# Kernel optimization log

Hardware: AMD Instinct MI355X
Metric: run time of the kernel (lower is better)

## Reference

```python
import jax, jax.numpy as jnp
import numpy as np

B, C, N, H = 16, 512, 4096, 512  # batch, visual_channels, visual_flat, hidden_size


def setup_inputs() -> dict:
    key = jax.random.key(0)
    kx, k1, k2, k3, k4 = jax.random.split(key, 5)
    stdv = 1.0 / np.sqrt(H)  # reset_parameters: uniform(-1/sqrt(size(0)), ...), size(0)=H for all weights
    u = lambda k, shape: jax.random.uniform(k, shape, jnp.float32, -stdv, stdv)
    return {
        "visual_inputs": jax.random.normal(kx, (B, C, N), jnp.float32),
        "w_cf": u(k1, (H, N)),  # channel_f: Linear(visual_flat -> hidden)
        "w_cg": u(k2, (H, N)),  # channel_g
        "w_sf": u(k3, (H, C)),  # spatial_f: Conv1d(C -> H, k=1), squeezed
        "w_sg": u(k4, (H, C)),  # spatial_g
    }


def reference(visual_inputs, w_cf, w_cg, w_sf, w_sg):
    x = visual_inputs  # [B, C, N]
    # ---- channel branch: sim[b,c,c'] = <cf[b,c,:], cg[b,c',:]>; summed over dim c then softmax over c'
    cf = jnp.einsum('bcn,hn->bch', x, w_cf)          # [B, C, H]
    cg = jnp.einsum('bcn,hn->bch', x, w_cg)          # [B, C, H]
    # sum_c sim[b,c,c'] = (sum_c cf[b,c,:]) . cg[b,c',:]  -- avoids [B,C,C]
    ch_comp = jnp.einsum('bh,bch->bc', cf.sum(axis=1), cg)        # [B, C]
    channel_mask = jax.nn.softmax(ch_comp, axis=1)[:, :, None]     # [B, C, 1]
    # ---- spatial branch: sim[b,i,j] = <sf[b,:,i], sg[b,:,j]>; summed over dim i then softmax over j
    sf = jnp.einsum('bcn,hc->bhn', x, w_sf)          # [B, H, N]
    sg = jnp.einsum('bcn,hc->bhn', x, w_sg)          # [B, H, N]
    sp_comp = jnp.einsum('bh,bhn->bn', sf.sum(axis=2), sg)         # [B, N]
    spatial_mask = jax.nn.softmax(sp_comp, axis=1)[:, None, :]     # [B, 1, N]
    outputs = x * channel_mask * spatial_mask        # [B, C, N]
    return outputs, channel_mask, spatial_mask
```

## Files before the change

### kernel.cpp

```cpp
#include <hip/hip_runtime.h>

#define Bq 16
#define Cq 512
#define Nq 4096
#define Hq 512

__global__ __launch_bounds__(256) void k1_xs(const float* __restrict__ x,
                                             float* __restrict__ xs_n,
                                             float* __restrict__ xs_c){
  __shared__ float lds[4];
  int blk = blockIdx.x;
  if (blk < Bq*4*4) {
    int b  = blk >> 4;
    int r  = blk & 15;
    int nc = r >> 2;
    int cc = r & 3;
    int n0 = nc*1024 + (int)threadIdx.x*4;
    const float4* px = (const float4*)(x + ((size_t)b*Cq + (size_t)cc*128)*Nq + n0);
    float4 acc = {0.f,0.f,0.f,0.f};
    #pragma unroll 4
    for (int c = 0; c < 128; ++c){
      float4 v = *px; px += Nq/4;
      acc.x += v.x; acc.y += v.y; acc.z += v.z; acc.w += v.w;
    }
    float* dst = xs_n + (size_t)b*Nq + n0;
    atomicAdd(dst+0, acc.x); atomicAdd(dst+1, acc.y);
    atomicAdd(dst+2, acc.z); atomicAdd(dst+3, acc.w);
  } else {
    int blk2 = blk - Bq*4*4;
    int b = blk2 >> 9;
    int c = blk2 & 511;
    const float4* row = (const float4*)(x + ((size_t)b*Cq + c)*Nq);
    float acc = 0.f;
    #pragma unroll
    for (int s = 0; s < 4; ++s){
      float4 v = row[s*256 + threadIdx.x];
      acc += (v.x + v.y) + (v.z + v.w);
    }
    #pragma unroll
    for (int off=32; off; off>>=1) acc += __shfl_down(acc, off, 64);
    if ((threadIdx.x & 63) == 0) lds[threadIdx.x >> 6] = acc;
    __syncthreads();
    if (threadIdx.x == 0) xs_c[b*Cq + c] = (lds[0]+lds[1])+(lds[2]+lds[3]);
  }
}

__global__ __launch_bounds__(256) void k2_s(const float* __restrict__ w_cf,
                                            const float* __restrict__ w_sf,
                                            const float* __restrict__ xs_n,
                                            const float* __restrict__ xs_c,
                                            float* __restrict__ s_cf,
                                            float* __restrict__ s_sf){
  __shared__ float lds[4];
  int blk = blockIdx.x;
  const float* w; const float* src; float* dst; int L;
  if (blk < Hq) { w = w_cf + (size_t)blk*Nq; src = xs_n; dst = s_cf; L = Nq; }
  else          { w = w_sf + (size_t)(blk-Hq)*Cq; src = xs_c; dst = s_sf; L = Cq; }
  int h = blk & (Hq-1);
  float acc[Bq];
  #pragma unroll
  for (int b=0;b<Bq;b++) acc[b]=0.f;
  for (int i = threadIdx.x; i < L; i += 256){
    float wv = w[i];
    #pragma unroll
    for (int b=0;b<Bq;b++) acc[b] += wv * src[b*L + i];
  }
  #pragma unroll
  for (int b=0;b<Bq;b++){
    float v = acc[b];
    #pragma unroll
    for (int off=32; off; off>>=1) v += __shfl_down(v, off, 64);
    if ((threadIdx.x & 63)==0) lds[threadIdx.x>>6] = v;
    __syncthreads();
    if (threadIdx.x==0) dst[b*Hq + h] = (lds[0]+lds[1])+(lds[2]+lds[3]);
    __syncthreads();
  }
}

__global__ __launch_bounds__(256) void k3_v(const float* __restrict__ w_cg,
                                            const float* __restrict__ w_sg,
                                            const float* __restrict__ s_cf,
                                            const float* __restrict__ s_sf,
                                            float* __restrict__ v_cg,
                                            float* __restrict__ v_sg){
  __shared__ float sl[Bq*64];
  int blk = blockIdx.x;
  const float* w; const float* s; float* dst; int L, jc, hc;
  if (blk < 128){ w=w_cg; s=s_cf; dst=v_cg; L=Nq; jc=blk>>3; hc=blk&7; }
  else { int k=blk-128; w=w_sg; s=s_sf; dst=v_sg; L=Cq; jc=k>>3; hc=k&7; }
  int h0 = hc*64;
  for (int i = threadIdx.x; i < Bq*64; i += 256){
    int b = i >> 6, hh = i & 63;
    sl[i] = s[b*Hq + h0 + hh];
  }
  __syncthreads();
  int j = (jc<<8) + (int)threadIdx.x;
  float acc[Bq];
  #pragma unroll
  for (int b=0;b<Bq;b++) acc[b]=0.f;
  for (int hh=0; hh<64; ++hh){
    float wv = w[(size_t)(h0+hh)*L + j];
    #pragma unroll
    for (int b=0;b<Bq;b++) acc[b] += sl[b*64+hh]*wv;
  }
  #pragma unroll
  for (int b=0;b<Bq;b++) atomicAdd(&dst[b*L + j], acc[b]);
}

__global__ __launch_bounds__(256) void k4_comp(const float* __restrict__ x,
                                               const float* __restrict__ v_cg,
                                               const float* __restrict__ v_sg,
                                               float* __restrict__ sp,
                                               float* __restrict__ ch){
  __shared__ float lds[4];
  int blk = blockIdx.x;
  if (blk < Bq*4*4){
    int b = blk >> 4; int r = blk & 15; int nc = r>>2; int cc = r&3;
    int n0 = nc*1024 + (int)threadIdx.x*4;
    const float4* px = (const float4*)(x + ((size_t)b*Cq + (size_t)cc*128)*Nq + n0);
    const float* vs = v_sg + b*Cq + cc*128;
    float4 acc = {0.f,0.f,0.f,0.f};
    #pragma unroll 4
    for (int c=0;c<128;++c){
      float4 v = *px; px += Nq/4;
      float s = vs[c];
      acc.x += v.x*s; acc.y += v.y*s; acc.z += v.z*s; acc.w += v.w*s;
    }
    float* dst = sp + (size_t)b*Nq + n0;
    atomicAdd(dst+0, acc.x); atomicAdd(dst+1, acc.y);
    atomicAdd(dst+2, acc.z); atomicAdd(dst+3, acc.w);
  } else {
    int blk2 = blk - Bq*4*4;
    int b = blk2 >> 9; int c = blk2 & 511;
    const float4* row = (const float4*)(x + ((size_t)b*Cq + c)*Nq);
    const float4* vg = (const float4*)(v_cg + (size_t)b*Nq);
    float acc=0.f;
    #pragma unroll
    for (int s=0;s<4;++s){
      float4 xv = row[s*256 + threadIdx.x];
      float4 vv = vg [s*256 + threadIdx.x];
      acc += xv.x*vv.x + xv.y*vv.y + xv.z*vv.z + xv.w*vv.w;
    }
    #pragma unroll
    for (int off=32; off; off>>=1) acc += __shfl_down(acc, off, 64);
    if ((threadIdx.x&63)==0) lds[threadIdx.x>>6]=acc;
    __syncthreads();
    if (threadIdx.x==0) ch[b*Cq+c] = (lds[0]+lds[1])+(lds[2]+lds[3]);
  }
}

__global__ __launch_bounds__(256) void k5_softmax(const float* __restrict__ ch,
                                                  const float* __restrict__ sp,
                                                  float* __restrict__ out){
  __shared__ float lds[4];
  __shared__ float bcast;
  int blk = blockIdx.x;
  const float* src; float* dst; int L;
  const size_t OUT0 = (size_t)Bq*Cq*Nq;
  if (blk < Bq){ int b=blk;    src=ch+(size_t)b*Cq; dst=out+OUT0+(size_t)b*Cq; L=Cq; }
  else         { int b=blk-Bq; src=sp+(size_t)b*Nq; dst=out+OUT0+(size_t)Bq*Cq+(size_t)b*Nq; L=Nq; }
  float m = -3.4e38f;
  for (int i=threadIdx.x;i<L;i+=256) m = fmaxf(m, src[i]);
  #pragma unroll
  for (int off=32; off; off>>=1) m = fmaxf(m, __shfl_down(m, off, 64));
  if ((threadIdx.x&63)==0) lds[threadIdx.x>>6]=m;
  __syncthreads();
  if (threadIdx.x==0) bcast = fmaxf(fmaxf(lds[0],lds[1]),fmaxf(lds[2],lds[3]));
  __syncthreads();
  m = bcast;
  float ssum=0.f;
  for (int i=threadIdx.x;i<L;i+=256) ssum += __expf(src[i]-m);
  #pragma unroll
  for (int off=32; off; off>>=1) ssum += __shfl_down(ssum, off, 64);
  __syncthreads();
  if ((threadIdx.x&63)==0) lds[threadIdx.x>>6]=ssum;
  __syncthreads();
  if (threadIdx.x==0) bcast = 1.f/((lds[0]+lds[1])+(lds[2]+lds[3]));
  __syncthreads();
  float inv = bcast;
  for (int i=threadIdx.x;i<L;i+=256) dst[i] = __expf(src[i]-m)*inv;
}

__global__ __launch_bounds__(256) void k6_out(const float* __restrict__ x,
                                              float* __restrict__ out){
  const size_t OUT0 = (size_t)Bq*Cq*Nq;
  const float* cm = out + OUT0;
  const float* sm = out + OUT0 + (size_t)Bq*Cq;
  int blk = blockIdx.x;
  int b = blk >> 11;
  int r = blk & 2047;
  int c = r >> 2;
  int q = r & 3;
  size_t rowoff = ((size_t)b*Cq + c)*Nq;
  int n0 = q*1024 + (int)threadIdx.x*4;
  float4 xv = *(const float4*)(x + rowoff + n0);
  float4 sv = *(const float4*)(sm + (size_t)b*Nq + n0);
  float cmv = cm[b*Cq + c];
  float4 o;
  o.x = xv.x*cmv*sv.x; o.y = xv.y*cmv*sv.y;
  o.z = xv.z*cmv*sv.z; o.w = xv.w*cmv*sv.w;
  *(float4*)(out + rowoff + n0) = o;
}

extern "C" void kernel_launch(void* const* d_in, const int* in_sizes, int n_in,
                              void* d_out, int out_size, void* d_ws, size_t ws_size,
                              hipStream_t stream){
  const float* x    = (const float*)d_in[0];
  const float* w_cf = (const float*)d_in[1];
  const float* w_cg = (const float*)d_in[2];
  const float* w_sf = (const float*)d_in[3];
  const float* w_sg = (const float*)d_in[4];
  float* out = (float*)d_out;

  float* ws   = (float*)d_ws;
  float* xs_n = ws;
  float* xs_c = xs_n + Bq*Nq;
  float* s_cf = xs_c + Bq*Cq;
  float* s_sf = s_cf + Bq*Hq;
  float* v_cg = s_sf + Bq*Hq;
  float* v_sg = v_cg + Bq*Nq;
  float* chc  = v_sg + Bq*Cq;
  float* spc  = chc  + Bq*Cq;

  size_t zbytes = (size_t)((spc + Bq*Nq) - ws) * sizeof(float);
  if (zbytes > ws_size) zbytes = ws_size;
  hipMemsetAsync(d_ws, 0, zbytes, stream);

  k1_xs     <<<Bq*4*4 + Bq*Cq, 256, 0, stream>>>(x, xs_n, xs_c);
  k2_s      <<<2*Hq,           256, 0, stream>>>(w_cf, w_sf, xs_n, xs_c, s_cf, s_sf);
  k3_v      <<<144,            256, 0, stream>>>(w_cg, w_sg, s_cf, s_sf, v_cg, v_sg);
  k4_comp   <<<Bq*4*4 + Bq*Cq, 256, 0, stream>>>(x, v_cg, v_sg, spc, chc);
  k5_softmax<<<2*Bq,           256, 0, stream>>>(chc, spc, out);
  k6_out    <<<Bq*Cq*4,        256, 0, stream>>>(x, out);
}
```

Before: 391.4 us.

## Fuse row and column reductions of x into single pass per kernel

Before, k1 and k4 each had two block populations that read x separately: one for column sums (over channels) and one for row sums (over spatial positions). Each of those kernels therefore streamed the 128MB input twice. Now each block takes 16 channel rows of one batch and computes both reductions from a single load, so each kernel reads x once. The workspace is reordered so that only the buffers written by atomics get zeroed. The trade-offs are fewer blocks (512), higher register pressure, and more atomics into xs_n and sp (32 contributions per element instead of 4).

After: 397.5 us. Within noise of the previous version (+1.5%).

```diff
diff --git a/kernel.cpp b/kernel.cpp
--- a/kernel.cpp
+++ b/kernel.cpp
@@ -5,44 +5,52 @@
 #define Nq 4096
 #define Hq 512
 
-__global__ __launch_bounds__(256) void k1_xs(const float* __restrict__ x,
-                                             float* __restrict__ xs_n,
-                                             float* __restrict__ xs_c){
-  __shared__ float lds[4];
-  int blk = blockIdx.x;
-  if (blk < Bq*4*4) {
-    int b  = blk >> 4;
-    int r  = blk & 15;
-    int nc = r >> 2;
-    int cc = r & 3;
-    int n0 = nc*1024 + (int)threadIdx.x*4;
-    const float4* px = (const float4*)(x + ((size_t)b*Cq + (size_t)cc*128)*Nq + n0);
-    float4 acc = {0.f,0.f,0.f,0.f};
-    #pragma unroll 4
-    for (int c = 0; c < 128; ++c){
-      float4 v = *px; px += Nq/4;
-      acc.x += v.x; acc.y += v.y; acc.z += v.z; acc.w += v.w;
+__global__ __launch_bounds__(256) void k1_stats(const float* __restrict__ x,
+                                                float* __restrict__ xs_n,
+                                                float* __restrict__ xs_c){
+  int blk = blockIdx.x;
+  int b  = blk >> 5;
+  int cc = blk & 31;
+  int c0 = cc << 4;
+  int t  = threadIdx.x;
+  const float4* base = (const float4*)(x + ((size_t)b*Cq + c0)*Nq);
+  float4 xn[4];
+  #pragma unroll
+  for (int k=0;k<4;++k){ xn[k].x=0.f; xn[k].y=0.f; xn[k].z=0.f; xn[k].w=0.f; }
+  float rs[16];
+  #pragma unroll
+  for (int r=0;r<16;++r){
+    const float4* row = base + (size_t)r*(Nq/4);
+    float rsum = 0.f;
+    #pragma unroll
+    for (int k=0;k<4;++k){
+      float4 v = row[t + (k<<8)];
+      xn[k].x += v.x; xn[k].y += v.y; xn[k].z += v.z; xn[k].w += v.w;
+      rsum += (v.x + v.y) + (v.z + v.w);
     }
-    float* dst = xs_n + (size_t)b*Nq + n0;
-    atomicAdd(dst+0, acc.x); atomicAdd(dst+1, acc.y);
-    atomicAdd(dst+2, acc.z); atomicAdd(dst+3, acc.w);
-  } else {
-    int blk2 = blk - Bq*4*4;
-    int b = blk2 >> 9;
-    int c = blk2 & 511;
-    const float4* row = (const float4*)(x + ((size_t)b*Cq + c)*Nq);
-    float acc = 0.f;
-    #pragma unroll
-    for (int s = 0; s < 4; ++s){
-      float4 v = row[s*256 + threadIdx.x];
-      acc += (v.x + v.y) + (v.z + v.w);
-    }
-    #pragma unroll
-    for (int off=32; off; off>>=1) acc += __shfl_down(acc, off, 64);
-    if ((threadIdx.x & 63) == 0) lds[threadIdx.x >> 6] = acc;
-    __syncthreads();
-    if (threadIdx.x == 0) xs_c[b*Cq + c] = (lds[0]+lds[1])+(lds[2]+lds[3]);
-  }
+    rs[r] = rsum;
+  }
+  float* dst = xs_n + (size_t)b*Nq + t*4;
+  #pragma unroll
+  for (int k=0;k<4;++k){
+    atomicAdd(dst + k*1024 + 0, xn[k].x);
+    atomicAdd(dst + k*1024 + 1, xn[k].y);
+    atomicAdd(dst + k*1024 + 2, xn[k].z);
+    atomicAdd(dst + k*1024 + 3, xn[k].w);
+  }
+  __shared__ float red[4][16];
+  int wave = t >> 6;
+  int lane = t & 63;
+  #pragma unroll
+  for (int r=0;r<16;++r){
+    float v = rs[r];
+    #pragma unroll
+    for (int off=32; off; off>>=1) v += __shfl_down(v, off, 64);
+    if (lane == 0) red[wave][r] = v;
+  }
+  __syncthreads();
+  if (t < 16)
+    xs_c[(size_t)b*Cq + c0 + t] = (red[0][t]+red[1][t])+(red[2][t]+red[3][t]);
 }
 
 __global__ __launch_bounds__(256) void k2_s(const float* __restrict__ w_cf,
@@ -112,41 +120,55 @@
                                                const float* __restrict__ v_sg,
                                                float* __restrict__ sp,
                                                float* __restrict__ ch){
-  __shared__ float lds[4];
-  int blk = blockIdx.x;
-  if (blk < Bq*4*4){
-    int b = blk >> 4; int r = blk & 15; int nc = r>>2; int cc = r&3;
-    int n0 = nc*1024 + (int)threadIdx.x*4;
-    const float4* px = (const float4*)(x + ((size_t)b*Cq + (size_t)cc*128)*Nq + n0);
-    const float* vs = v_sg + b*Cq + cc*128;
-    float4 acc = {0.f,0.f,0.f,0.f};
-    #pragma unroll 4
-    for (int c=0;c<128;++c){
-      float4 v = *px; px += Nq/4;
-      float s = vs[c];
-      acc.x += v.x*s; acc.y += v.y*s; acc.z += v.z*s; acc.w += v.w*s;
+  int blk = blockIdx.x;
+  int b  = blk >> 5;
+  int cc = blk & 31;
+  int c0 = cc << 4;
+  int t  = threadIdx.x;
+  const float4* base = (const float4*)(x + ((size_t)b*Cq + c0)*Nq);
+  const float4* vgp  = (const float4*)(v_cg + (size_t)b*Nq);
+  float4 vg[4];
+  #pragma unroll
+  for (int k=0;k<4;++k) vg[k] = vgp[t + (k<<8)];
+  float4 spa[4];
+  #pragma unroll
+  for (int k=0;k<4;++k){ spa[k].x=0.f; spa[k].y=0.f; spa[k].z=0.f; spa[k].w=0.f; }
+  float rs[16];
+  #pragma unroll
+  for (int r=0;r<16;++r){
+    const float4* row = base + (size_t)r*(Nq/4);
+    float vsr = v_sg[(size_t)b*Cq + c0 + r];
+    float rsum = 0.f;
+    #pragma unroll
+    for (int k=0;k<4;++k){
+      float4 v = row[t + (k<<8)];
+      rsum += v.x*vg[k].x + v.y*vg[k].y + v.z*vg[k].z + v.w*vg[k].w;
+      spa[k].x += v.x*vsr; spa[k].y += v.y*vsr;
+      spa[k].z += v.z*vsr; spa[k].w += v.w*vsr;
     }
-    float* dst = sp + (size_t)b*Nq + n0;
-    atomicAdd(dst+0, acc.x); atomicAdd(dst+1, acc.y);
-    atomicAdd(dst+2, acc.z); atomicAdd(dst+3, acc.w);
-  } else {
-    int blk2 = blk - Bq*4*4;
-    int b = blk2 >> 9; int c = blk2 & 511;
-    const float4* row = (const float4*)(x + ((size_t)b*Cq + c)*Nq);
-    const float4* vg = (const float4*)(v_cg + (size_t)b*Nq);
-    float acc=0.f;
-    #pragma unroll
-    for (int s=0;s<4;++s){
-      float4 xv = row[s*256 + threadIdx.x];
-      float4 vv = vg [s*256 + threadIdx.x];
-      acc += xv.x*vv.x + xv.y*vv.y + xv.z*vv.z + xv.w*vv.w;
-    }
-    #pragma unroll
-    for (int off=32; off; off>>=1) acc += __shfl_down(acc, off, 64);
-    if ((threadIdx.x&63)==0) lds[threadIdx.x>>6]=acc;
-    __syncthreads();
-    if (threadIdx.x==0) ch[b*Cq+c] = (lds[0]+lds[1])+(lds[2]+lds[3]);
-  }
+    rs[r] = rsum;
+  }
+  float* dst = sp + (size_t)b*Nq + t*4;
+  #pragma unroll
+  for (int k=0;k<4;++k){
+    atomicAdd(dst + k*1024 + 0, spa[k].x);
+    atomicAdd(dst + k*1024 + 1, spa[k].y);
+    atomicAdd(dst + k*1024 + 2, spa[k].z);
+    atomicAdd(dst + k*1024 + 3, spa[k].w);
+  }
+  __shared__ float red[4][16];
+  int wave = t >> 6;
+  int lane = t & 63;
+  #pragma unroll
+  for (int r=0;r<16;++r){
+    float v = rs[r];
+    #pragma unroll
+    for (int off=32; off; off>>=1) v += __shfl_down(v, off, 64);
+    if (lane == 0) red[wave][r] = v;
+  }
+  __syncthreads();
+  if (t < 16)
+    ch[(size_t)b*Cq + c0 + t] = (red[0][t]+red[1][t])+(red[2][t]+red[3][t]);
 }
 
 __global__ __launch_bounds__(256) void k5_softmax(const float* __restrict__ ch,
@@ -214,22 +236,22 @@
 
   float* ws   = (float*)d_ws;
   float* xs_n = ws;
-  float* xs_c = xs_n + Bq*Nq;
+  float* v_cg = xs_n + Bq*Nq;
+  float* v_sg = v_cg + Bq*Nq;
+  float* spc  = v_sg + Bq*Cq;
+  float* xs_c = spc  + Bq*Nq;
   float* s_cf = xs_c + Bq*Cq;
   float* s_sf = s_cf + Bq*Hq;
-  float* v_cg = s_sf + Bq*Hq;
-  float* v_sg = v_cg + Bq*Nq;
-  float* chc  = v_sg + Bq*Cq;
-  float* spc  = chc  + Bq*Cq;
-
-  size_t zbytes = (size_t)((spc + Bq*Nq) - ws) * sizeof(float);
+  float* chc  = s_sf + Bq*Hq;
+
+  size_t zbytes = (size_t)(Bq*Nq + Bq*Nq + Bq*Cq + Bq*Nq) * sizeof(float);
   if (zbytes > ws_size) zbytes = ws_size;
   hipMemsetAsync(d_ws, 0, zbytes, stream);
 
-  k1_xs     <<<Bq*4*4 + Bq*Cq, 256, 0, stream>>>(x, xs_n, xs_c);
-  k2_s      <<<2*Hq,           256, 0, stream>>>(w_cf, w_sf, xs_n, xs_c, s_cf, s_sf);
-  k3_v      <<<144,            256, 0, stream>>>(w_cg, w_sg, s_cf, s_sf, v_cg, v_sg);
-  k4_comp   <<<Bq*4*4 + Bq*Cq, 256, 0, stream>>>(x, v_cg, v_sg, spc, chc);
-  k5_softmax<<<2*Bq,           256, 0, stream>>>(chc, spc, out);
-  k6_out    <<<Bq*Cq*4,        256, 0, stream>>>(x, out);
-}
+  k1_stats  <<<Bq*32,   256, 0, stream>>>(x, xs_n, xs_c);
+  k2_s      <<<2*Hq,    256, 0, stream>>>(w_cf, w_sf, xs_n, xs_c, s_cf, s_sf);
+  k3_v      <<<144,     256, 0, stream>>>(w_cg, w_sg, s_cf, s_sf, v_cg, v_sg);
+  k4_comp   <<<Bq*32,   256, 0, stream>>>(x, v_cg, v_sg, spc, chc);
+  k5_softmax<<<2*Bq,    256, 0, stream>>>(chc, spc, out);
+  k6_out    <<<Bq*Cq*4, 256, 0, stream>>>(x, out);
+}
```

## Replace atomic accumulation with deterministic partial sums and drop workspace memset

Applied to the files above, without the earlier changes.

The column-sum and spatial-comp paths now have each thread reduce over all 512 channels and store the result directly, with no float atomics. k3_v writes per-head-chunk partial results that a new k3b_red kernel sums, so the workspace memset is no longer needed. This removes the atomic traffic and the memset launch. In exchange it adds one kernel launch, and the channel reductions run on fewer, longer threads with scalar rather than float4 loads.

Measured after the change: 365.8 us. -6.5%, faster.

```diff
diff --git a/kernel.cpp b/kernel.cpp
--- a/kernel.cpp
+++ b/kernel.cpp
@@ -5,29 +5,22 @@
 #define Nq 4096
 #define Hq 512
 
-__global__ __launch_bounds__(256) void k1_xs(const float* __restrict__ x,
-                                             float* __restrict__ xs_n,
-                                             float* __restrict__ xs_c){
-  __shared__ float lds[4];
-  int blk = blockIdx.x;
-  if (blk < Bq*4*4) {
+__global__ __launch_bounds__(256) void k1_stats(const float* __restrict__ x,
+                                                float* __restrict__ xs_n,
+                                                float* __restrict__ xs_c){
+  int blk = blockIdx.x;
+  if (blk < 256){
     int b  = blk >> 4;
-    int r  = blk & 15;
-    int nc = r >> 2;
-    int cc = r & 3;
-    int n0 = nc*1024 + (int)threadIdx.x*4;
-    const float4* px = (const float4*)(x + ((size_t)b*Cq + (size_t)cc*128)*Nq + n0);
-    float4 acc = {0.f,0.f,0.f,0.f};
-    #pragma unroll 4
-    for (int c = 0; c < 128; ++c){
-      float4 v = *px; px += Nq/4;
-      acc.x += v.x; acc.y += v.y; acc.z += v.z; acc.w += v.w;
-    }
-    float* dst = xs_n + (size_t)b*Nq + n0;
-    atomicAdd(dst+0, acc.x); atomicAdd(dst+1, acc.y);
-    atomicAdd(dst+2, acc.z); atomicAdd(dst+3, acc.w);
+    int nc = blk & 15;
+    int n  = (nc << 8) + (int)threadIdx.x;
+    const float* p = x + (size_t)b*Cq*Nq + n;
+    float acc = 0.f;
+    #pragma unroll 16
+    for (int c = 0; c < Cq; ++c) acc += p[(size_t)c*Nq];
+    xs_n[(size_t)b*Nq + n] = acc;
   } else {
-    int blk2 = blk - Bq*4*4;
+    __shared__ float lds[4];
+    int blk2 = blk - 256;
     int b = blk2 >> 9;
     int c = blk2 & 511;
     const float4* row = (const float4*)(x + ((size_t)b*Cq + c)*Nq);
@@ -41,7 +34,7 @@
     for (int off=32; off; off>>=1) acc += __shfl_down(acc, off, 64);
     if ((threadIdx.x & 63) == 0) lds[threadIdx.x >> 6] = acc;
     __syncthreads();
-    if (threadIdx.x == 0) xs_c[b*Cq + c] = (lds[0]+lds[1])+(lds[2]+lds[3]);
+    if (threadIdx.x == 0) xs_c[(size_t)b*Cq + c] = (lds[0]+lds[1])+(lds[2]+lds[3]);
   }
 }
 
@@ -81,13 +74,13 @@
                                             const float* __restrict__ w_sg,
                                             const float* __restrict__ s_cf,
                                             const float* __restrict__ s_sf,
-                                            float* __restrict__ v_cg,
-                                            float* __restrict__ v_sg){
+                                            float* __restrict__ part_cg,
+                                            float* __restrict__ part_sg){
   __shared__ float sl[Bq*64];
   int blk = blockIdx.x;
   const float* w; const float* s; float* dst; int L, jc, hc;
-  if (blk < 128){ w=w_cg; s=s_cf; dst=v_cg; L=Nq; jc=blk>>3; hc=blk&7; }
-  else { int k=blk-128; w=w_sg; s=s_sf; dst=v_sg; L=Cq; jc=k>>3; hc=k&7; }
+  if (blk < 128){ w=w_cg; s=s_cf; dst=part_cg; L=Nq; jc=blk>>3; hc=blk&7; }
+  else { int k=blk-128; w=w_sg; s=s_sf; dst=part_sg; L=Cq; jc=k>>3; hc=k&7; }
   int h0 = hc*64;
   for (int i = threadIdx.x; i < Bq*64; i += 256){
     int b = i >> 6, hh = i & 63;
@@ -104,7 +97,27 @@
     for (int b=0;b<Bq;b++) acc[b] += sl[b*64+hh]*wv;
   }
   #pragma unroll
-  for (int b=0;b<Bq;b++) atomicAdd(&dst[b*L + j], acc[b]);
+  for (int b=0;b<Bq;b++) dst[((size_t)hc*Bq + b)*L + j] = acc[b];
+}
+
+__global__ __launch_bounds__(256) void k3b_red(const float* __restrict__ part_cg,
+                                               const float* __restrict__ part_sg,
+                                               float* __restrict__ v_cg,
+                                               float* __restrict__ v_sg){
+  int blk = blockIdx.x;
+  if (blk < 256){
+    int i = (blk << 8) + (int)threadIdx.x;
+    float acc = 0.f;
+    #pragma unroll
+    for (int hc=0; hc<8; ++hc) acc += part_cg[(size_t)hc*(Bq*Nq) + i];
+    v_cg[i] = acc;
+  } else {
+    int i = ((blk-256) << 8) + (int)threadIdx.x;
+    float acc = 0.f;
+    #pragma unroll
+    for (int hc=0; hc<8; ++hc) acc += part_sg[(size_t)hc*(Bq*Cq) + i];
+    v_sg[i] = acc;
+  }
 }
 
 __global__ __launch_bounds__(256) void k4_comp(const float* __restrict__ x,
@@ -112,40 +125,36 @@
                                                const float* __restrict__ v_sg,
                                                float* __restrict__ sp,
                                                float* __restrict__ ch){
-  __shared__ float lds[4];
-  int blk = blockIdx.x;
-  if (blk < Bq*4*4){
-    int b = blk >> 4; int r = blk & 15; int nc = r>>2; int cc = r&3;
-    int n0 = nc*1024 + (int)threadIdx.x*4;
-    const float4* px = (const float4*)(x + ((size_t)b*Cq + (size_t)cc*128)*Nq + n0);
-    const float* vs = v_sg + b*Cq + cc*128;
-    float4 acc = {0.f,0.f,0.f,0.f};
-    #pragma unroll 4
-    for (int c=0;c<128;++c){
-      float4 v = *px; px += Nq/4;
-      float s = vs[c];
-      acc.x += v.x*s; acc.y += v.y*s; acc.z += v.z*s; acc.w += v.w*s;
-    }
-    float* dst = sp + (size_t)b*Nq + n0;
-    atomicAdd(dst+0, acc.x); atomicAdd(dst+1, acc.y);
-    atomicAdd(dst+2, acc.z); atomicAdd(dst+3, acc.w);
+  int blk = blockIdx.x;
+  if (blk < 256){
+    int b  = blk >> 4;
+    int nc = blk & 15;
+    int n  = (nc << 8) + (int)threadIdx.x;
+    const float* p  = x + (size_t)b*Cq*Nq + n;
+    const float* vs = v_sg + (size_t)b*Cq;
+    float acc = 0.f;
+    #pragma unroll 16
+    for (int c = 0; c < Cq; ++c) acc += p[(size_t)c*Nq] * vs[c];
+    sp[(size_t)b*Nq + n] = acc;
   } else {
-    int blk2 = blk - Bq*4*4;
-    int b = blk2 >> 9; int c = blk2 & 511;
+    __shared__ float lds[4];
+    int blk2 = blk - 256;
+    int b = blk2 >> 9;
+    int c = blk2 & 511;
     const float4* row = (const float4*)(x + ((size_t)b*Cq + c)*Nq);
-    const float4* vg = (const float4*)(v_cg + (size_t)b*Nq);
-    float acc=0.f;
-    #pragma unroll
-    for (int s=0;s<4;++s){
+    const float4* vg  = (const float4*)(v_cg + (size_t)b*Nq);
+    float acc = 0.f;
+    #pragma unroll
+    for (int s = 0; s < 4; ++s){
       float4 xv = row[s*256 + threadIdx.x];
       float4 vv = vg [s*256 + threadIdx.x];
       acc += xv.x*vv.x + xv.y*vv.y + xv.z*vv.z + xv.w*vv.w;
     }
     #pragma unroll
     for (int off=32; off; off>>=1) acc += __shfl_down(acc, off, 64);
-    if ((threadIdx.x&63)==0) lds[threadIdx.x>>6]=acc;
-    __syncthreads();
-    if (threadIdx.x==0) ch[b*Cq+c] = (lds[0]+lds[1])+(lds[2]+lds[3]);
+    if ((threadIdx.x & 63) == 0) lds[threadIdx.x >> 6] = acc;
+    __syncthreads();
+    if (threadIdx.x == 0) ch[(size_t)b*Cq + c] = (lds[0]+lds[1])+(lds[2]+lds[3]);
   }
 }
 
@@ -212,24 +221,23 @@
   const float* w_sg = (const float*)d_in[4];
   float* out = (float*)d_out;
 
-  float* ws   = (float*)d_ws;
-  float* xs_n = ws;
-  float* xs_c = xs_n + Bq*Nq;
-  float* s_cf = xs_c + Bq*Cq;
-  float* s_sf = s_cf + Bq*Hq;
-  float* v_cg = s_sf + Bq*Hq;
-  float* v_sg = v_cg + Bq*Nq;
-  float* chc  = v_sg + Bq*Cq;
-  float* spc  = chc  + Bq*Cq;
-
-  size_t zbytes = (size_t)((spc + Bq*Nq) - ws) * sizeof(float);
-  if (zbytes > ws_size) zbytes = ws_size;
-  hipMemsetAsync(d_ws, 0, zbytes, stream);
-
-  k1_xs     <<<Bq*4*4 + Bq*Cq, 256, 0, stream>>>(x, xs_n, xs_c);
-  k2_s      <<<2*Hq,           256, 0, stream>>>(w_cf, w_sf, xs_n, xs_c, s_cf, s_sf);
-  k3_v      <<<144,            256, 0, stream>>>(w_cg, w_sg, s_cf, s_sf, v_cg, v_sg);
-  k4_comp   <<<Bq*4*4 + Bq*Cq, 256, 0, stream>>>(x, v_cg, v_sg, spc, chc);
-  k5_softmax<<<2*Bq,           256, 0, stream>>>(chc, spc, out);
-  k6_out    <<<Bq*Cq*4,        256, 0, stream>>>(x, out);
-}
+  float* ws      = (float*)d_ws;
+  float* xs_n    = ws;
+  float* xs_c    = xs_n    + Bq*Nq;
+  float* s_cf    = xs_c    + Bq*Cq;
+  float* s_sf    = s_cf    + Bq*Hq;
+  float* part_cg = s_sf    + Bq*Hq;
+  float* part_sg = part_cg + 8*Bq*Nq;
+  float* v_cg    = part_sg + 8*Bq*Cq;
+  float* v_sg    = v_cg    + Bq*Nq;
+  float* chc     = v_sg    + Bq*Cq;
+  float* spc     = chc     + Bq*Cq;
+
+  k1_stats  <<<256 + Bq*Cq, 256, 0, stream>>>(x, xs_n, xs_c);
+  k2_s      <<<2*Hq,        256, 0, stream>>>(w_cf, w_sf, xs_n, xs_c, s_cf, s_sf);
+  k3_v      <<<144,         256, 0, stream>>>(w_cg, w_sg, s_cf, s_sf, part_cg, part_sg);
+  k3b_red   <<<288,         256, 0, stream>>>(part_cg, part_sg, v_cg, v_sg);
+  k4_comp   <<<256 + Bq*Cq, 256, 0, stream>>>(x, v_cg, v_sg, spc, chc);
+  k5_softmax<<<2*Bq,        256, 0, stream>>>(chc, spc, out);
+  k6_out    <<<Bq*Cq*4,     256, 0, stream>>>(x, out);
+}
```
